# Performance work log

Measured on AMD Instinct MI355X. Metric: run time of the kernel, lower is better.

The kernel has to match this reference:

```python
import jax, jax.numpy as jnp
import numpy as np

TEMP = 0.7
TOPK_RATIO = 0.75
BN_EPS = 1e-5  # eval-mode BN with running_mean=0, running_var=1


def conv3x3(x, w):
    # x: [N,C,H,W], w: [O,I,3,3], stride 1, pad 1
    return jax.lax.conv_general_dilated(x, w, (1, 1), 'SAME',
                                        dimension_numbers=('NCHW', 'OIHW', 'NCHW'))


def bn(x, g, b):
    scale = g / jnp.sqrt(1.0 + BN_EPS)
    return x * scale[:, None, None] + b[:, None, None]


def glu(x):
    c = x.shape[1] // 2
    return x[:, :c] * jax.nn.sigmoid(x[:, c:])


def resblock(x, w1, g1, b1, w2, g2, b2):
    out = glu(bn(conv3x3(x, w1), g1, b1))
    out = bn(conv3x3(out, w2), g2, b2)
    return out + x


def refined_attention(h_code, word_embs, w_ctx, mask):
    B, C, H, W = h_code.shape
    Q = H * W
    S = word_embs.shape[2]
    # conv_context is a 1x1 conv (no bias): pure channel projection
    sourceT = jnp.einsum('oc,bcs->bos', w_ctx, word_embs)   # [B, idf, S]
    target = h_code.reshape(B, C, Q)                        # [B, idf, Q]
    attn = jnp.einsum('bcq,bcs->bqs', target, sourceT)      # [B, Q, S]
    attn = attn.reshape(B * Q, S) / TEMP
    # faithful to torch: mask.repeat(queryL, 1) tiles mask over rows
    mask_exp = jnp.tile(mask, (Q, 1))                       # [B*Q, S]
    attn = jnp.where(mask_exp, -jnp.inf, attn)
    if TOPK_RATIO < 1.0 and S > 1:
        k = max(1, int(S * TOPK_RATIO))
        topk_vals, _ = jax.lax.top_k(attn, k)               # sorted desc
        threshold = topk_vals[:, -1:]                       # min of top-k
        attn = jnp.where(attn < threshold, -jnp.inf, attn)
    p = jax.nn.softmax(attn, axis=1)
    nan_rows = jnp.any(jnp.isnan(p), axis=1, keepdims=True)
    p = jnp.where(nan_rows, 1.0 / S, p)                     # uniform fallback
    p = p.reshape(B, Q, S)
    attn_t = jnp.swapaxes(p, 1, 2)                          # [B, S, Q]
    wctx = jnp.einsum('bos,bsq->boq', sourceT, attn_t).reshape(B, C, H, W)
    att_map = attn_t.reshape(B, S, H, W)
    return wctx, att_map


def upsample2x(x):
    return jnp.repeat(jnp.repeat(x, 2, axis=2), 2, axis=3)


def reference(h_code, c_code, word_embs, w_ctx,
              r0_w1, r0_g1, r0_b1, r0_w2, r0_g2, r0_b2,
              r1_w1, r1_g1, r1_b1, r1_w2, r1_g2, r1_b2,
              up_w, up_g, up_b, mask):
    # c_code is in the signature of NEXT_STAGE_G.forward but unused (as in AttnGAN)
    c_code_att, att = refined_attention(h_code, word_embs, w_ctx, mask)
    h_c = jnp.concatenate([h_code, c_code_att], axis=1)     # [B, 2*ngf, H, W]
    out = resblock(h_c, r0_w1, r0_g1, r0_b1, r0_w2, r0_g2, r0_b2)
    out = resblock(out, r1_w1, r1_g1, r1_b1, r1_w2, r1_g2, r1_b2)
    # upBlock: nearest upsample x2 -> conv3x3(2ngf, 2ngf) -> BN -> GLU -> ngf
    out = glu(bn(conv3x3(upsample2x(out), up_w), up_g, up_b))
    return out, att


def setup_inputs() -> dict:
    key = jax.random.key(0)
    ks = jax.random.split(key, 24)
    B, ngf, H, W = 8, 64, 128, 128
    nef, ncf, S = 256, 100, 32
    C2 = 2 * ngf  # 128
    std = 0.02
    inp = {
        'h_code': jax.random.normal(ks[0], (B, ngf, H, W), jnp.float32),
        'c_code': jax.random.normal(ks[1], (B, ncf), jnp.float32),
        'word_embs': jax.random.normal(ks[2], (B, nef, S), jnp.float32),
        'mask': jax.random.randint(ks[3], (B, S), 0, 2).astype(bool),
        'w_ctx': jax.random.normal(ks[4], (ngf, nef), jnp.float32) * std,
    }
    for i, base in enumerate([5, 11]):
        inp[f'r{i}_w1'] = jax.random.normal(ks[base + 0], (2 * C2, C2, 3, 3), jnp.float32) * std
        inp[f'r{i}_g1'] = jnp.ones((2 * C2,), jnp.float32)
        inp[f'r{i}_b1'] = jnp.zeros((2 * C2,), jnp.float32)
        inp[f'r{i}_w2'] = jax.random.normal(ks[base + 3], (C2, C2, 3, 3), jnp.float32) * std
        inp[f'r{i}_g2'] = jnp.ones((C2,), jnp.float32)
        inp[f'r{i}_b2'] = jnp.zeros((C2,), jnp.float32)
    inp['up_w'] = jax.random.normal(ks[17], (2 * ngf, C2, 3, 3), jnp.float32) * std
    inp['up_g'] = jnp.ones((2 * ngf,), jnp.float32)
    inp['up_b'] = jnp.zeros((2 * ngf,), jnp.float32)
    return inp
```

## Files before the change

kernel.cpp:

```cpp
#include <hip/hip_runtime.h>
#include <math.h>


#define B_N 8
#define NGF 64
#define HC 128
#define WC 128
#define QN (HC*WC)
#define NEF 256
#define SN 32
#define TEMP_INV (1.0f/0.7f)
#define BN_SC 0.99999500003749969f
#define TOPK 24

typedef _Float16 f16;
typedef __attribute__((ext_vector_type(8))) _Float16 f16x8;
typedef __attribute__((ext_vector_type(4))) _Float16 f16x4;
typedef __attribute__((ext_vector_type(4))) float f32x4;

__device__ __forceinline__ void gload16(const void* g, void* l) {
    __builtin_amdgcn_global_load_lds(
        (const __attribute__((address_space(1))) void*)g,
        (__attribute__((address_space(3))) void*)l,
        16, 0, 0);
}

__global__ void prep_mask_k(const void* __restrict__ mraw,
                            unsigned* __restrict__ mbits,
                            unsigned* __restrict__ zp) {
    __shared__ int mode;
    if (threadIdx.x == 0) {
        const unsigned* u = (const unsigned*)mraw;
        bool i32 = true, f32m = true;
        for (int i = 0; i < 64; ++i) {
            unsigned v = u[i];
            if (v > 1u) i32 = false;
            if (v != 0u && v != 0x3F800000u) f32m = false;
        }
        mode = i32 ? 0 : (f32m ? 1 : 2);
    }
    __syncthreads();
    int t = threadIdx.x;
    if (t < 64) zp[(t >> 4) * 262144 + (t & 15)] = 0u;
    if (t < B_N) {
        unsigned bits = 0;
        for (int s = 0; s < SN; ++s) {
            int idx = t * SN + s;
            bool on;
            if (mode == 0)      on = ((const int*)mraw)[idx] != 0;
            else if (mode == 1) on = ((const float*)mraw)[idx] != 0.0f;
            else                on = ((const unsigned char*)mraw)[idx] != 0;
            if (on) bits |= (1u << s);
        }
        mbits[t] = bits;
    }
}

__global__ __launch_bounds__(256) void source_t_k(
        const float* __restrict__ w_ctx, const float* __restrict__ word_embs,
        float* __restrict__ sT) {
    int b = blockIdx.x >> 3;
    int o = ((blockIdx.x & 7) << 3) + (threadIdx.x >> 5);
    int s = threadIdx.x & 31;
    const float* wrow = w_ctx + (size_t)o * NEF;
    const float* wb = word_embs + (size_t)b * NEF * SN + s;
    float acc = 0.0f;
    #pragma unroll 8
    for (int c = 0; c < NEF; ++c) acc += wrow[c] * wb[(size_t)c * SN];
    sT[((size_t)b * NGF + o) * SN + s] = acc;
}

__global__ __launch_bounds__(256) void attention_k(
        const float* __restrict__ h_code, const float* __restrict__ sT,
        const unsigned* __restrict__ mbits,
        float* __restrict__ att_out,
        f16* __restrict__ hc) {
    int r0 = blockIdx.x * 256;
    int b = r0 >> 14;
    __shared__ float st[NGF * SN];
    const float* stg = sT + (size_t)b * NGF * SN;
    for (int i = threadIdx.x; i < NGF * SN; i += 256) st[i] = stg[i];
    __syncthreads();
    int q = (r0 & (QN - 1)) + threadIdx.x;

    const float* hb = h_code + (size_t)b * NGF * QN + q;
    f16* hcb = hc + (size_t)b * QN * 128;

    float a[SN];
    #pragma unroll
    for (int s = 0; s < SN; ++s) a[s] = 0.0f;
    for (int g8 = 0; g8 < 8; ++g8) {
        f16x8 t;
        #pragma unroll
        for (int r = 0; r < 8; ++r) {
            float v = hb[(size_t)(g8 * 8 + r) * QN];
            t[r] = (f16)v;
            #pragma unroll
            for (int s = 0; s < SN; ++s) a[s] += v * st[(g8 * 8 + r) * SN + s];
        }
        *(f16x8*)(hcb + ((size_t)g8 * QN + q) * 8) = t;
    }
    unsigned mb = mbits[q & 7];
    #pragma unroll
    for (int s = 0; s < SN; ++s)
        a[s] = ((mb >> s) & 1u) ? -INFINITY : a[s] * TEMP_INV;

    float thr = -INFINITY;
    #pragma unroll
    for (int s = 0; s < SN; ++s) {
        int rank = 0;
        #pragma unroll
        for (int j = 0; j < SN; ++j)
            rank += (a[j] > a[s]) || (a[j] == a[s] && j < s);
        if (rank == TOPK - 1) thr = a[s];
    }
    float m = -INFINITY;
    #pragma unroll
    for (int s = 0; s < SN; ++s) {
        if (a[s] < thr) a[s] = -INFINITY;
        m = fmaxf(m, a[s]);
    }
    float p[SN];
    if (m == -INFINITY) {
        #pragma unroll
        for (int s = 0; s < SN; ++s) p[s] = 1.0f / SN;
    } else {
        float sum = 0.0f;
        #pragma unroll
        for (int s = 0; s < SN; ++s) { p[s] = __expf(a[s] - m); sum += p[s]; }
        float inv = 1.0f / sum;
        #pragma unroll
        for (int s = 0; s < SN; ++s) p[s] *= inv;
    }
    float* ao = att_out + (size_t)b * SN * QN + q;
    #pragma unroll
    for (int s = 0; s < SN; ++s) ao[(size_t)s * QN] = p[s];
    for (int g8 = 0; g8 < 8; ++g8) {
        f16x8 t;
        #pragma unroll
        for (int r = 0; r < 8; ++r) {
            float acc = 0.0f;
            #pragma unroll
            for (int s = 0; s < SN; ++s) acc += st[(g8 * 8 + r) * SN + s] * p[s];
            t[r] = (f16)acc;
        }
        *(f16x8*)(hcb + ((size_t)(8 + g8) * QN + q) * 8) = t;
    }
}

__global__ __launch_bounds__(256) void wt_transform_k(
        const float* __restrict__ w, f16* __restrict__ wt,
        int total, int HALF ) {
    int idx = blockIdx.x * 256 + threadIdx.x;
    if (idx >= total) return;
    int e   = idx & 7;
    int gp  = (idx >> 3) & 3;
    int cop = (idx >> 5) & 63;
    int u   = idx >> 11;
    int t   = u % 9;
    int v   = u / 9;
    int cc  = v & 3;
    int cb  = v >> 2;
    int g   = gp ^ ((cop >> 1) & 3);
    int ci  = cc * 32 + g * 8 + e;
    int co  = HALF ? (cop < 32 ? cb * 32 + cop : HALF + cb * 32 + (cop - 32))
                   : cb * 64 + cop;
    wt[idx] = (f16)w[((size_t)co * 128 + ci) * 9 + t];
}

__global__ __launch_bounds__(256) void wt_up_transform_k(
        const float* __restrict__ w, f16* __restrict__ wt) {
    int idx = blockIdx.x * 256 + threadIdx.x;
    int e   = idx & 7;
    int gp  = (idx >> 3) & 3;
    int cop = (idx >> 5) & 63;
    int tap = (idx >> 11) & 3;
    int pw  = (idx >> 13) & 1;
    int cc  = (idx >> 14) & 3;
    int ph  = (idx >> 16) & 1;
    int cb  = (idx >> 17) & 1;
    int g   = gp ^ ((cop >> 1) & 3);
    int ci  = cc * 32 + g * 8 + e;
    int co  = cop < 32 ? cb * 32 + cop : 64 + cb * 32 + (cop - 32);
    int ra = tap >> 1, bb = tap & 1;
    const float* wp = w + ((size_t)co * 128 + ci) * 9;
    float acc = 0.0f;
    #pragma unroll
    for (int kh = 0; kh < 3; ++kh) {
        int rma = (ph == 0) ? (kh == 0 ? 0 : 1) : (kh == 2 ? 1 : 0);
        if (rma != ra) continue;
        #pragma unroll
        for (int kw = 0; kw < 3; ++kw) {
            int cma = (pw == 0) ? (kw == 0 ? 0 : 1) : (kw == 2 ? 1 : 0);
            if (cma == bb) acc += wp[kh * 3 + kw];
        }
    }
    wt[idx] = (f16)acc;
}

template<int COUT, bool GLU, bool RES, int HOUT, int WOUT>
__global__ __launch_bounds__(256) void conv_mfma_k(
        const f16* __restrict__ in, const f16* __restrict__ wt,
        const float* __restrict__ gamma, const float* __restrict__ beta,
        const f16* __restrict__ res, f16* __restrict__ outh,
        const char* __restrict__ zeros) {
    constexpr int HALF = COUT / 2;
    constexpr int OCH  = GLU ? HALF : COUT;
    constexpr int HIN  = HOUT;
    constexpr int WIN  = WOUT;
    constexpr int RPT  = 256 / WOUT;
    constexpr int ROWS_IN = RPT + 2;
    constexpr int NIN_G   = ROWS_IN * 520;
    constexpr int NIN_IT  = (NIN_G + 255) / 256;
    constexpr int NIN_PAD = NIN_IT * 256;
    constexpr int WBYTES  = 36864;
    constexpr int WIT     = 9;

    __shared__ char smem[NIN_PAD * 16 + WBYTES];
    char* sW = smem + NIN_PAD * 16;

    const int tid = threadIdx.x, lane = tid & 63, wv = tid >> 6;
    const int l15 = lane & 15, kg = lane >> 4;
    const int b = blockIdx.z, cb = blockIdx.y, qt = blockIdx.x;
    const int q0 = qt * 256;
    const int h0 = q0 / WOUT;

    f32x4 acc[4][4];
    #pragma unroll
    for (int m = 0; m < 4; ++m)
        #pragma unroll
        for (int n = 0; n < 4; ++n) acc[m][n] = (f32x4){0.f, 0.f, 0.f, 0.f};

    const f16* inb = in + (size_t)b * HIN * WIN * 128;
    const char* wtb = (const char*)wt + (size_t)cb * 147456;

    const char* srcK[NIN_IT];
    #pragma unroll
    for (int k = 0; k < NIN_IT; ++k) {
        int idx = (k << 8) + tid;
        int r = idx / 520;
        int rem = idx - r * 520;
        int wi = rem >> 2, gp = rem & 3;
        int g = gp ^ ((wi >> 1) & 3);
        int gh = h0 - 1 + r;
        int gw = wi - 1;
        const char* s = zeros;
        if (r < ROWS_IN && (unsigned)gh < (unsigned)HOUT && (unsigned)gw < (unsigned)WOUT)
            s = (const char*)(inb + (((size_t)g * (HIN * WIN) + (size_t)gh * WIN + gw) << 3));
        srcK[k] = s;
    }
    const int dstB = (tid & 192) << 4;

    for (int cc = 0; cc < 4; ++cc) {
        #pragma unroll
        for (int k = 0; k < NIN_IT; ++k)
            gload16(srcK[k] + (cc << 20), smem + (k << 12) + dstB);
        const char* wsrc = wtb + cc * WBYTES + (tid << 4);
        #pragma unroll
        for (int k = 0; k < WIT; ++k)
            gload16(wsrc + (k << 12), sW + (k << 12) + dstB);
        __syncthreads();

        #pragma unroll
        for (int t = 0; t < 9; ++t) {
            f16x8 af[4], bf[4];
            #pragma unroll
            for (int m = 0; m < 4; ++m) {
                int co = m * 16 + l15;
                af[m] = *(const f16x8*)(sW + (t << 12) + (co << 6)
                                        + ((kg ^ ((co >> 1) & 3)) << 4));
            }
            #pragma unroll
            for (int n = 0; n < 4; ++n) {
                const int kh = t / 3, kw = t % 3;
                int row = (wv >> 1) + kh;
                int wi = ((wv & 1) << 6) + (n << 4) + l15 + kw;
                int off = row * 8320 + wi * 64 + ((kg ^ ((wi >> 1) & 3)) << 4);
                bf[n] = *(const f16x8*)(smem + off);
            }
            #pragma unroll
            for (int m = 0; m < 4; ++m)
                #pragma unroll
                for (int n = 0; n < 4; ++n)
                    acc[m][n] = __builtin_amdgcn_mfma_f32_16x16x32_f16(af[m], bf[n], acc[m][n], 0, 0, 0);
        }
        __syncthreads();
    }

    const int r4 = kg * 4;
    if (GLU) {
        #pragma unroll
        for (int mv = 0; mv < 2; ++mv) {
            const int v0 = cb * 32 + mv * 16 + r4;
            float s1[4], o1[4], s2[4], o2[4];
            #pragma unroll
            for (int r = 0; r < 4; ++r) {
                s1[r] = gamma[v0 + r] * BN_SC;        o1[r] = beta[v0 + r];
                s2[r] = gamma[v0 + r + HALF] * BN_SC; o2[r] = beta[v0 + r + HALF];
            }
            #pragma unroll
            for (int n = 0; n < 4; ++n) {
                float ov[4];
                #pragma unroll
                for (int r = 0; r < 4; ++r) {
                    float yv = acc[mv][n][r] * s1[r] + o1[r];
                    float zv = acc[mv + 2][n][r] * s2[r] + o2[r];
                    ov[r] = yv / (1.0f + __expf(-zv));
                }
                const int qc = (wv << 6) + (n << 4) + l15;
                f16x4 tv;
                #pragma unroll
                for (int r = 0; r < 4; ++r) tv[r] = (f16)ov[r];
                *(f16x4*)(outh + ((((size_t)b * (OCH / 8) + (v0 >> 3)) << 14)
                                  + q0 + qc) * 8 + (v0 & 7)) = tv;
            }
        }
    } else {
        #pragma unroll
        for (int m = 0; m < 4; ++m) {
            const int c0 = cb * 64 + m * 16 + r4;
            float s[4], o[4];
            #pragma unroll
            for (int r = 0; r < 4; ++r) {
                s[r] = gamma[c0 + r] * BN_SC; o[r] = beta[c0 + r];
            }
            #pragma unroll
            for (int n = 0; n < 4; ++n) {
                const int qc = (wv << 6) + (n << 4) + l15;
                const size_t gaddr = ((((size_t)b * 16 + (c0 >> 3)) << 14) + q0 + qc) * 8 + (c0 & 7);
                float ov[4];
                #pragma unroll
                for (int r = 0; r < 4; ++r) ov[r] = acc[m][n][r] * s[r] + o[r];
                if (RES) {
                    f16x4 rv = *(const f16x4*)(res + gaddr);
                    #pragma unroll
                    for (int r = 0; r < 4; ++r) ov[r] += (float)rv[r];
                }
                f16x4 tv;
                #pragma unroll
                for (int r = 0; r < 4; ++r) tv[r] = (f16)ov[r];
                *(f16x4*)(outh + gaddr) = tv;
            }
        }
    }
}

__global__ __launch_bounds__(512, 1) void conv_up_k(
        const f16* __restrict__ in, const f16* __restrict__ wt,
        const float* __restrict__ gamma, const float* __restrict__ beta,
        float* __restrict__ outf, const char* __restrict__ zeros) {
    constexpr int HIN = 128, WIN = 128;
    constexpr int BUFB = 24960 + 32768;
    __shared__ char smem[2 * BUFB];

    const int tid = threadIdx.x, lane = tid & 63, wv = tid >> 6;
    const int l15 = lane & 15, kg = lane >> 4;
    const int b = blockIdx.z, cb = blockIdx.y;
    const int j = blockIdx.x >> 1, ph = blockIdx.x & 1;
    const int rr = wv >> 2;
    const int p  = (wv >> 1) & 1;
    const int jq = ((wv & 1) << 6) + l15;

    f32x4 acc[4][4];
    #pragma unroll
    for (int m = 0; m < 4; ++m)
        #pragma unroll
        for (int n = 0; n < 4; ++n) acc[m][n] = (f32x4){0.f, 0.f, 0.f, 0.f};

    const f16* inb = in + (size_t)b * HIN * WIN * 128;
    const char* wtb = (const char*)wt + (size_t)(cb * 2 + ph) * 131072;

    const char* srcK[4];
    #pragma unroll
    for (int k = 0; k < 4; ++k) {
        int idx = (k < 3) ? ((k << 9) + tid) : (1536 + tid);
        int r = idx / 520;
        int rem = idx - r * 520;
        int wi = rem >> 2, gp = rem & 3;
        int g = gp ^ ((wi >> 1) & 3);
        int sh = 2 * j - 1 + ph + r;
        int sw = wi - 1;
        const char* s = zeros;
        if (r < 3 && (unsigned)sh < (unsigned)HIN && (unsigned)sw < (unsigned)WIN)
            s = (const char*)(inb + (((size_t)g * (HIN * WIN) + (size_t)sh * WIN + sw) << 3));
        srcK[k] = s;
    }
    const int dstB = (tid & 448) << 4;

    auto stage = [&](int cc, int buf) {
        char* base = smem + buf * BUFB;
        #pragma unroll
        for (int k = 0; k < 3; ++k)
            gload16(srcK[k] + (cc << 20), base + (k << 13) + dstB);
        if (tid < 24)
            gload16(srcK[3] + (cc << 20), base + 24576);
        const char* wsrc = wtb + cc * 32768 + (tid << 4);
        #pragma unroll
        for (int k = 0; k < 4; ++k)
            gload16(wsrc + (k << 13), base + 24960 + (k << 13) + dstB);
    };

    stage(0, 0);
    __syncthreads();
    for (int cc = 0; cc < 4; ++cc) {
        if (cc < 3) stage(cc + 1, (cc + 1) & 1);
        const char* bb = smem + (cc & 1) * BUFB;
        const char* wB = bb + 24960;

        #pragma unroll
        for (int t = 0; t < 4; ++t) {
            f16x8 af[4], bf[4];
            const int tapbase = (p * 4 + t) << 12;
            #pragma unroll
            for (int m = 0; m < 4; ++m) {
                int co = m * 16 + l15;
                af[m] = *(const f16x8*)(wB + tapbase + (co << 6)
                                        + ((kg ^ ((co >> 1) & 3)) << 4));
            }
            #pragma unroll
            for (int n = 0; n < 4; ++n) {
                int si = jq + (n << 4) + (t & 1) + p;
                int off = (rr + (t >> 1)) * 8320 + si * 64
                          + ((kg ^ ((si >> 1) & 3)) << 4);
                bf[n] = *(const f16x8*)(bb + off);
            }
            #pragma unroll
            for (int m = 0; m < 4; ++m)
                #pragma unroll
                for (int n = 0; n < 4; ++n)
                    acc[m][n] = __builtin_amdgcn_mfma_f32_16x16x32_f16(af[m], bf[n], acc[m][n], 0, 0, 0);
        }
        __syncthreads();
    }

    const int r4 = kg * 4;
    const int h = 4 * j + 2 * rr + ph;
    #pragma unroll
    for (int mv = 0; mv < 2; ++mv) {
        const int v0 = cb * 32 + mv * 16 + r4;
        float s1[4], o1[4], s2[4], o2[4];
        #pragma unroll
        for (int r = 0; r < 4; ++r) {
            s1[r] = gamma[v0 + r] * BN_SC;      o1[r] = beta[v0 + r];
            s2[r] = gamma[v0 + r + 64] * BN_SC; o2[r] = beta[v0 + r + 64];
        }
        #pragma unroll
        for (int n = 0; n < 4; ++n) {
            const int w = 2 * (jq + (n << 4)) + p;
            float ov[4];
            #pragma unroll
            for (int r = 0; r < 4; ++r) {
                float yv = acc[mv][n][r] * s1[r] + o1[r];
                float zv = acc[mv + 2][n][r] * s2[r] + o2[r];
                ov[r] = yv / (1.0f + __expf(-zv));
            }
            #pragma unroll
            for (int r = 0; r < 4; ++r)
                outf[(((size_t)b * 64 + v0 + r) * 256 + h) * 256 + w] = ov[r];
        }
    }
}

extern "C" void kernel_launch(void* const* d_in, const int* in_sizes, int n_in,
                              void* d_out, int out_size, void* d_ws, size_t ws_size,
                              hipStream_t stream) {
    (void)in_sizes; (void)n_in; (void)out_size; (void)ws_size;
    const float* h_code    = (const float*)d_in[0];
    const float* word_embs = (const float*)d_in[2];
    const void*  mask      = d_in[3];
    const float* w_ctx     = (const float*)d_in[4];
    const float* r0_w1 = (const float*)d_in[5];
    const float* r0_g1 = (const float*)d_in[6];
    const float* r0_b1 = (const float*)d_in[7];
    const float* r0_w2 = (const float*)d_in[8];
    const float* r0_g2 = (const float*)d_in[9];
    const float* r0_b2 = (const float*)d_in[10];
    const float* r1_w1 = (const float*)d_in[11];
    const float* r1_g1 = (const float*)d_in[12];
    const float* r1_b1 = (const float*)d_in[13];
    const float* r1_w2 = (const float*)d_in[14];
    const float* r1_g2 = (const float*)d_in[15];
    const float* r1_b2 = (const float*)d_in[16];
    const float* up_w  = (const float*)d_in[17];
    const float* up_g  = (const float*)d_in[18];
    const float* up_b  = (const float*)d_in[19];

    float* outp = (float*)d_out;
    float* attp = outp + (size_t)B_N * NGF * 4 * HC * WC;

    unsigned* mbits = (unsigned*)d_ws;
    float* sT  = (float*)((char*)d_ws + 1024);
    char* zeros = (char*)d_ws + ((size_t)4 << 20);
    f16* hcA   = (f16*)((char*)d_ws + ((size_t)8 << 20));
    f16* wtbuf = (f16*)((char*)d_ws + ((size_t)40 << 20));

    const int W1_TOT = 4 * 4 * 9 * 64 * 32;
    const int W2_TOT = 2 * 4 * 9 * 64 * 32;
    const int WUP_TOT = 2 * 2 * 4 * 2 * 4 * 64 * 32;
    f16* Wr0c1 = wtbuf;
    f16* Wr0c2 = Wr0c1 + W1_TOT;
    f16* Wr1c1 = Wr0c2 + W2_TOT;
    f16* Wr1c2 = Wr1c1 + W1_TOT;
    f16* Wup   = Wr1c2 + W2_TOT;

    f16* Bbuf = (f16*)d_out;
    f16* Cbuf = (f16*)((char*)d_out + ((size_t)32 << 20));

    prep_mask_k<<<1, 64, 0, stream>>>(mask, mbits, (unsigned*)zeros);
    source_t_k<<<64, 256, 0, stream>>>(w_ctx, word_embs, sT);

    wt_transform_k<<<(W1_TOT + 255) / 256, 256, 0, stream>>>(r0_w1, Wr0c1, W1_TOT, 128);
    wt_transform_k<<<(W2_TOT + 255) / 256, 256, 0, stream>>>(r0_w2, Wr0c2, W2_TOT, 0);
    wt_transform_k<<<(W1_TOT + 255) / 256, 256, 0, stream>>>(r1_w1, Wr1c1, W1_TOT, 128);
    wt_transform_k<<<(W2_TOT + 255) / 256, 256, 0, stream>>>(r1_w2, Wr1c2, W2_TOT, 0);
    wt_up_transform_k<<<WUP_TOT / 256, 256, 0, stream>>>(up_w, Wup);

    attention_k<<<(B_N * QN) / 256, 256, 0, stream>>>(h_code, sT, mbits, attp, hcA);

    conv_mfma_k<256, true,  false, 128, 128>
        <<<dim3(64, 4, B_N), 256, 0, stream>>>(hcA, Wr0c1, r0_g1, r0_b1, nullptr, Bbuf, zeros);
    conv_mfma_k<128, false, true,  128, 128>
        <<<dim3(64, 2, B_N), 256, 0, stream>>>(Bbuf, Wr0c2, r0_g2, r0_b2, hcA, Cbuf, zeros);
    conv_mfma_k<256, true,  false, 128, 128>
        <<<dim3(64, 4, B_N), 256, 0, stream>>>(Cbuf, Wr1c1, r1_g1, r1_b1, nullptr, Bbuf, zeros);
    conv_mfma_k<128, false, true,  128, 128>
        <<<dim3(64, 2, B_N), 256, 0, stream>>>(Bbuf, Wr1c2, r1_g2, r1_b2, Cbuf, hcA, zeros);
    conv_up_k<<<dim3(128, 2, B_N), 512, 0, stream>>>(hcA, Wup, up_g, up_b, outp, zeros);
}
```

Measured before the change: 395.1 us.

## Split upsample conv blocks by output column parity to shrink LDS and raise occupancy

The upsample conv kernel now gives each block a single output-column parity (pcol), so grid.x doubles. Each block stages only half the weights, in a single 16KB LDS buffer instead of double-buffered 32KB, and each wave keeps 2x4 accumulators instead of 4x4. Launch bounds move to 4 blocks per SM so more blocks can be resident. In exchange, input rows are loaded twice across the two parity blocks, and weight staging is now serialized behind an extra barrier each chunk instead of being overlapped with compute.

```diff
diff --git a/kernel.cpp b/kernel.cpp
--- a/kernel.cpp
+++ b/kernel.cpp
@@ -345,30 +345,32 @@
     }
 }
 
-__global__ __launch_bounds__(512, 1) void conv_up_k(
+__global__ __launch_bounds__(512, 4) void conv_up_k(
         const f16* __restrict__ in, const f16* __restrict__ wt,
         const float* __restrict__ gamma, const float* __restrict__ beta,
         float* __restrict__ outf, const char* __restrict__ zeros) {
     constexpr int HIN = 128, WIN = 128;
-    constexpr int BUFB = 24960 + 32768;
-    __shared__ char smem[2 * BUFB];
+    constexpr int INB = 24960;
+    __shared__ char smem[2 * INB + 16384];
+    char* wB = smem + 2 * INB;
 
     const int tid = threadIdx.x, lane = tid & 63, wv = tid >> 6;
     const int l15 = lane & 15, kg = lane >> 4;
     const int b = blockIdx.z, cb = blockIdx.y;
-    const int j = blockIdx.x >> 1, ph = blockIdx.x & 1;
+    const int j = blockIdx.x >> 2, ph = (blockIdx.x >> 1) & 1, pcol = blockIdx.x & 1;
     const int rr = wv >> 2;
-    const int p  = (wv >> 1) & 1;
-    const int jq = ((wv & 1) << 6) + l15;
-
-    f32x4 acc[4][4];
-    #pragma unroll
-    for (int m = 0; m < 4; ++m)
+    const int ch = (wv >> 1) & 1;
+    const int mh = wv & 1;
+
+    f32x4 acc[2][4];
+    #pragma unroll
+    for (int m = 0; m < 2; ++m)
         #pragma unroll
         for (int n = 0; n < 4; ++n) acc[m][n] = (f32x4){0.f, 0.f, 0.f, 0.f};
 
     const f16* inb = in + (size_t)b * HIN * WIN * 128;
-    const char* wtb = (const char*)wt + (size_t)(cb * 2 + ph) * 131072;
+    const char* wtb = (const char*)wt + (size_t)(cb * 2 + ph) * 131072
+                      + pcol * 16384;
 
     const char* srcK[4];
     #pragma unroll
@@ -387,77 +389,78 @@
     }
     const int dstB = (tid & 448) << 4;
 
-    auto stage = [&](int cc, int buf) {
-        char* base = smem + buf * BUFB;
+    auto stage_in = [&](int cc, int buf) {
+        char* base = smem + buf * INB;
         #pragma unroll
         for (int k = 0; k < 3; ++k)
             gload16(srcK[k] + (cc << 20), base + (k << 13) + dstB);
         if (tid < 24)
             gload16(srcK[3] + (cc << 20), base + 24576);
+    };
+    auto stage_w = [&](int cc) {
         const char* wsrc = wtb + cc * 32768 + (tid << 4);
         #pragma unroll
-        for (int k = 0; k < 4; ++k)
-            gload16(wsrc + (k << 13), base + 24960 + (k << 13) + dstB);
+        for (int k = 0; k < 2; ++k)
+            gload16(wsrc + (k << 13), wB + (k << 13) + dstB);
     };
 
-    stage(0, 0);
+    stage_in(0, 0);
+    stage_w(0);
     __syncthreads();
     for (int cc = 0; cc < 4; ++cc) {
-        if (cc < 3) stage(cc + 1, (cc + 1) & 1);
-        const char* bb = smem + (cc & 1) * BUFB;
-        const char* wB = bb + 24960;
+        if (cc < 3) stage_in(cc + 1, (cc + 1) & 1);
+        const char* bb = smem + (cc & 1) * INB;
 
         #pragma unroll
         for (int t = 0; t < 4; ++t) {
-            f16x8 af[4], bf[4];
-            const int tapbase = (p * 4 + t) << 12;
-            #pragma unroll
-            for (int m = 0; m < 4; ++m) {
-                int co = m * 16 + l15;
-                af[m] = *(const f16x8*)(wB + tapbase + (co << 6)
+            f16x8 af[2], bf[4];
+            #pragma unroll
+            for (int m = 0; m < 2; ++m) {
+                int co = (mh + m * 2) * 16 + l15;
+                af[m] = *(const f16x8*)(wB + (t << 12) + (co << 6)
                                         + ((kg ^ ((co >> 1) & 3)) << 4));
             }
             #pragma unroll
             for (int n = 0; n < 4; ++n) {
-                int si = jq + (n << 4) + (t & 1) + p;
+                int si = ch * 64 + (n << 4) + l15 + (t & 1) + pcol;
                 int off = (rr + (t >> 1)) * 8320 + si * 64
                           + ((kg ^ ((si >> 1) & 3)) << 4);
                 bf[n] = *(const f16x8*)(bb + off);
             }
             #pragma unroll
-            for (int m = 0; m < 4; ++m)
+            for (int m = 0; m < 2; ++m)
                 #pragma unroll
                 for (int n = 0; n < 4; ++n)
                     acc[m][n] = __builtin_amdgcn_mfma_f32_16x16x32_f16(af[m], bf[n], acc[m][n], 0, 0, 0);
         }
         __syncthreads();
-    }
-
-    const int r4 = kg * 4;
+        if (cc < 3) {
+            stage_w(cc + 1);
+            __syncthreads();
+        }
+    }
+
+    const int v0 = cb * 32 + mh * 16 + kg * 4;
     const int h = 4 * j + 2 * rr + ph;
-    #pragma unroll
-    for (int mv = 0; mv < 2; ++mv) {
-        const int v0 = cb * 32 + mv * 16 + r4;
-        float s1[4], o1[4], s2[4], o2[4];
+    float s1[4], o1[4], s2[4], o2[4];
+    #pragma unroll
+    for (int r = 0; r < 4; ++r) {
+        s1[r] = gamma[v0 + r] * BN_SC;      o1[r] = beta[v0 + r];
+        s2[r] = gamma[v0 + r + 64] * BN_SC; o2[r] = beta[v0 + r + 64];
+    }
+    #pragma unroll
+    for (int n = 0; n < 4; ++n) {
+        const int w = 2 * (ch * 64 + (n << 4) + l15) + pcol;
+        float ov[4];
         #pragma unroll
         for (int r = 0; r < 4; ++r) {
-            s1[r] = gamma[v0 + r] * BN_SC;      o1[r] = beta[v0 + r];
-            s2[r] = gamma[v0 + r + 64] * BN_SC; o2[r] = beta[v0 + r + 64];
-        }
-        #pragma unroll
-        for (int n = 0; n < 4; ++n) {
-            const int w = 2 * (jq + (n << 4)) + p;
-            float ov[4];
-            #pragma unroll
-            for (int r = 0; r < 4; ++r) {
-                float yv = acc[mv][n][r] * s1[r] + o1[r];
-                float zv = acc[mv + 2][n][r] * s2[r] + o2[r];
-                ov[r] = yv / (1.0f + __expf(-zv));
-            }
-            #pragma unroll
-            for (int r = 0; r < 4; ++r)
-                outf[(((size_t)b * 64 + v0 + r) * 256 + h) * 256 + w] = ov[r];
-        }
+            float yv = acc[0][n][r] * s1[r] + o1[r];
+            float zv = acc[1][n][r] * s2[r] + o2[r];
+            ov[r] = yv / (1.0f + __expf(-zv));
+        }
+        #pragma unroll
+        for (int r = 0; r < 4; ++r)
+            outf[(((size_t)b * 64 + v0 + r) * 256 + h) * 256 + w] = ov[r];
     }
 }
 
@@ -525,5 +528,5 @@
         <<<dim3(64, 4, B_N), 256, 0, stream>>>(Cbuf, Wr1c1, r1_g1, r1_b1, nullptr, Bbuf, zeros);
     conv_mfma_k<128, false, true,  128, 128>
         <<<dim3(64, 2, B_N), 256, 0, stream>>>(Bbuf, Wr1c2, r1_g2, r1_b2, Cbuf, hcA, zeros);
-    conv_up_k<<<dim3(128, 2, B_N), 512, 0, stream>>>(hcA, Wup, up_g, up_b, outp, zeros);
-}
+    conv_up_k<<<dim3(256, 2, B_N), 512, 0, stream>>>(hcA, Wup, up_g, up_b, outp, zeros);
+}
```

Result: slower. 414.5 us (+4.9%).

## Double-buffer input tiles and enlarge conv blocks to 512 threads

Applied to the files above, without the earlier changes.

The 3x3 MFMA conv kernel now processes four output rows per block with 512 threads and double-buffers the input halo tile in LDS. The next channel chunk's input is prefetched while the current chunk computes, and weights are reloaded after a barrier. The aim is to hide global-to-LDS latency and share each weight tile across more output positions. In exchange LDS use rises to about 150 KB per block, which limits occupancy to one block per CU, and extra barriers remain around the weight reloads.

```diff
diff --git a/kernel.cpp b/kernel.cpp
--- a/kernel.cpp
+++ b/kernel.cpp
@@ -198,32 +198,25 @@
     wt[idx] = (f16)acc;
 }
 
-template<int COUT, bool GLU, bool RES, int HOUT, int WOUT>
-__global__ __launch_bounds__(256) void conv_mfma_k(
+template<int COUT, bool GLU, bool RES>
+__global__ __launch_bounds__(512) void conv_mfma_k(
         const f16* __restrict__ in, const f16* __restrict__ wt,
         const float* __restrict__ gamma, const float* __restrict__ beta,
         const f16* __restrict__ res, f16* __restrict__ outh,
         const char* __restrict__ zeros) {
     constexpr int HALF = COUT / 2;
     constexpr int OCH  = GLU ? HALF : COUT;
-    constexpr int HIN  = HOUT;
-    constexpr int WIN  = WOUT;
-    constexpr int RPT  = 256 / WOUT;
-    constexpr int ROWS_IN = RPT + 2;
-    constexpr int NIN_G   = ROWS_IN * 520;
-    constexpr int NIN_IT  = (NIN_G + 255) / 256;
-    constexpr int NIN_PAD = NIN_IT * 256;
-    constexpr int WBYTES  = 36864;
-    constexpr int WIT     = 9;
-
-    __shared__ char smem[NIN_PAD * 16 + WBYTES];
-    char* sW = smem + NIN_PAD * 16;
+    constexpr int IBUF = 57344;
+
+    __shared__ char smem[2 * IBUF + 36864];
+    char* wB = smem + 2 * IBUF;
 
     const int tid = threadIdx.x, lane = tid & 63, wv = tid >> 6;
     const int l15 = lane & 15, kg = lane >> 4;
     const int b = blockIdx.z, cb = blockIdx.y, qt = blockIdx.x;
-    const int q0 = qt * 256;
-    const int h0 = q0 / WOUT;
+    const int q0 = qt * 512;
+    const int h0 = qt * 4;
+    const int lr = wv >> 1, chf = wv & 1;
 
     f32x4 acc[4][4];
     #pragma unroll
@@ -231,13 +224,13 @@
         #pragma unroll
         for (int n = 0; n < 4; ++n) acc[m][n] = (f32x4){0.f, 0.f, 0.f, 0.f};
 
-    const f16* inb = in + (size_t)b * HIN * WIN * 128;
+    const f16* inb = in + (size_t)b * QN * 128;
     const char* wtb = (const char*)wt + (size_t)cb * 147456;
 
-    const char* srcK[NIN_IT];
-    #pragma unroll
-    for (int k = 0; k < NIN_IT; ++k) {
-        int idx = (k << 8) + tid;
+    const char* srcK[7];
+    #pragma unroll
+    for (int k = 0; k < 7; ++k) {
+        int idx = (k << 9) + tid;
         int r = idx / 520;
         int rem = idx - r * 520;
         int wi = rem >> 2, gp = rem & 3;
@@ -245,38 +238,49 @@
         int gh = h0 - 1 + r;
         int gw = wi - 1;
         const char* s = zeros;
-        if (r < ROWS_IN && (unsigned)gh < (unsigned)HOUT && (unsigned)gw < (unsigned)WOUT)
-            s = (const char*)(inb + (((size_t)g * (HIN * WIN) + (size_t)gh * WIN + gw) << 3));
+        if (r < 6 && (unsigned)gh < (unsigned)HC && (unsigned)gw < (unsigned)WC)
+            s = (const char*)(inb + (((size_t)g * QN + (size_t)gh * WC + gw) << 3));
         srcK[k] = s;
     }
-    const int dstB = (tid & 192) << 4;
-
+    const int dstB = (tid & 448) << 4;
+
+    auto stage_in = [&](int cc, int buf) {
+        char* base = smem + buf * IBUF;
+        #pragma unroll
+        for (int k = 0; k < 7; ++k)
+            gload16(srcK[k] + (cc << 20), base + (k << 13) + dstB);
+    };
+    auto stage_w = [&](int cc) {
+        const char* wsrc = wtb + cc * 36864 + (tid << 4);
+        #pragma unroll
+        for (int k = 0; k < 4; ++k)
+            gload16(wsrc + (k << 13), wB + (k << 13) + dstB);
+        if (tid < 256)
+            gload16(wsrc + (4 << 13), wB + (4 << 13) + dstB);
+    };
+
+    stage_in(0, 0);
+    stage_w(0);
+    __syncthreads();
     for (int cc = 0; cc < 4; ++cc) {
-        #pragma unroll
-        for (int k = 0; k < NIN_IT; ++k)
-            gload16(srcK[k] + (cc << 20), smem + (k << 12) + dstB);
-        const char* wsrc = wtb + cc * WBYTES + (tid << 4);
-        #pragma unroll
-        for (int k = 0; k < WIT; ++k)
-            gload16(wsrc + (k << 12), sW + (k << 12) + dstB);
-        __syncthreads();
+        if (cc < 3) stage_in(cc + 1, (cc + 1) & 1);
+        const char* bb = smem + (cc & 1) * IBUF;
 
         #pragma unroll
         for (int t = 0; t < 9; ++t) {
+            const int kh = t / 3, kw = t % 3;
             f16x8 af[4], bf[4];
             #pragma unroll
             for (int m = 0; m < 4; ++m) {
                 int co = m * 16 + l15;
-                af[m] = *(const f16x8*)(sW + (t << 12) + (co << 6)
+                af[m] = *(const f16x8*)(wB + (t << 12) + (co << 6)
                                         + ((kg ^ ((co >> 1) & 3)) << 4));
             }
             #pragma unroll
             for (int n = 0; n < 4; ++n) {
-                const int kh = t / 3, kw = t % 3;
-                int row = (wv >> 1) + kh;
-                int wi = ((wv & 1) << 6) + (n << 4) + l15 + kw;
-                int off = row * 8320 + wi * 64 + ((kg ^ ((wi >> 1) & 3)) << 4);
-                bf[n] = *(const f16x8*)(smem + off);
+                int wi = chf * 64 + (n << 4) + l15 + kw;
+                int off = (lr + kh) * 8320 + wi * 64 + ((kg ^ ((wi >> 1) & 3)) << 4);
+                bf[n] = *(const f16x8*)(bb + off);
             }
             #pragma unroll
             for (int m = 0; m < 4; ++m)
@@ -285,9 +289,14 @@
                     acc[m][n] = __builtin_amdgcn_mfma_f32_16x16x32_f16(af[m], bf[n], acc[m][n], 0, 0, 0);
         }
         __syncthreads();
+        if (cc < 3) {
+            stage_w(cc + 1);
+            __syncthreads();
+        }
     }
 
     const int r4 = kg * 4;
+    const int qb = lr * 128 + chf * 64;
     if (GLU) {
         #pragma unroll
         for (int mv = 0; mv < 2; ++mv) {
@@ -300,6 +309,7 @@
             }
             #pragma unroll
             for (int n = 0; n < 4; ++n) {
+                const int qc = qb + (n << 4) + l15;
                 float ov[4];
                 #pragma unroll
                 for (int r = 0; r < 4; ++r) {
@@ -307,7 +317,6 @@
                     float zv = acc[mv + 2][n][r] * s2[r] + o2[r];
                     ov[r] = yv / (1.0f + __expf(-zv));
                 }
-                const int qc = (wv << 6) + (n << 4) + l15;
                 f16x4 tv;
                 #pragma unroll
                 for (int r = 0; r < 4; ++r) tv[r] = (f16)ov[r];
@@ -326,7 +335,7 @@
             }
             #pragma unroll
             for (int n = 0; n < 4; ++n) {
-                const int qc = (wv << 6) + (n << 4) + l15;
+                const int qc = qb + (n << 4) + l15;
                 const size_t gaddr = ((((size_t)b * 16 + (c0 >> 3)) << 14) + q0 + qc) * 8 + (c0 & 7);
                 float ov[4];
                 #pragma unroll
@@ -517,13 +526,13 @@
 
     attention_k<<<(B_N * QN) / 256, 256, 0, stream>>>(h_code, sT, mbits, attp, hcA);
 
-    conv_mfma_k<256, true,  false, 128, 128>
-        <<<dim3(64, 4, B_N), 256, 0, stream>>>(hcA, Wr0c1, r0_g1, r0_b1, nullptr, Bbuf, zeros);
-    conv_mfma_k<128, false, true,  128, 128>
-        <<<dim3(64, 2, B_N), 256, 0, stream>>>(Bbuf, Wr0c2, r0_g2, r0_b2, hcA, Cbuf, zeros);
-    conv_mfma_k<256, true,  false, 128, 128>
-        <<<dim3(64, 4, B_N), 256, 0, stream>>>(Cbuf, Wr1c1, r1_g1, r1_b1, nullptr, Bbuf, zeros);
-    conv_mfma_k<128, false, true,  128, 128>
-        <<<dim3(64, 2, B_N), 256, 0, stream>>>(Bbuf, Wr1c2, r1_g2, r1_b2, Cbuf, hcA, zeros);
+    conv_mfma_k<256, true,  false>
+        <<<dim3(32, 4, B_N), 512, 0, stream>>>(hcA, Wr0c1, r0_g1, r0_b1, nullptr, Bbuf, zeros);
+    conv_mfma_k<128, false, true>
+        <<<dim3(32, 2, B_N), 512, 0, stream>>>(Bbuf, Wr0c2, r0_g2, r0_b2, hcA, Cbuf, zeros);
+    conv_mfma_k<256, true,  false>
+        <<<dim3(32, 4, B_N), 512, 0, stream>>>(Cbuf, Wr1c1, r1_g1, r1_b1, nullptr, Bbuf, zeros);
+    conv_mfma_k<128, false, true>
+        <<<dim3(32, 2, B_N), 512, 0, stream>>>(Bbuf, Wr1c2, r1_g2, r1_b2, Cbuf, hcA, zeros);
     conv_up_k<<<dim3(128, 2, B_N), 512, 0, stream>>>(hcA, Wup, up_g, up_b, outp, zeros);
 }
```

Result: no change. 394.1 us, median of 2 (-0.3%).
